# Kernel tuning notes

Hardware: AMD Instinct MI355X
Metric: run time of the kernel (lower is better)

Reference implementation:

```python
import jax, jax.numpy as jnp
import numpy as np

TEMPERATURE = 0.07
MARGIN = 0.15
HARD_NEG_RATIO = 0.5


def setup_inputs() -> dict:
    key = jax.random.key(0)
    k1, k2, k3 = jax.random.split(key, 3)
    B, D = 4096, 128
    drug_emb = jax.random.normal(k1, (B, D), dtype=jnp.float32)
    se_emb = jax.random.normal(k2, (B, D), dtype=jnp.float32)
    # labels spread over [0, 5) so that |diff| > 1.0 negatives exist
    labels = jax.random.uniform(k3, (B,), dtype=jnp.float32) * 5.0
    return {"drug_emb": drug_emb, "se_emb": se_emb, "labels": labels}


def _single_branch_loss(z, labels):
    B = z.shape[0]
    # F.normalize(z, dim=-1): divide by norm clamped to eps
    z = z / jnp.maximum(jnp.linalg.norm(z, axis=-1, keepdims=True), 1e-12)
    sim = jnp.matmul(z, z.T) / TEMPERATURE                      # [B, B]
    label_diff = jnp.abs(labels[None, :] - labels[:, None])     # [B, B]
    self_mask = ~jnp.eye(B, dtype=bool)
    pos_weight = jnp.exp(-label_diff / MARGIN) * self_mask      # soft positives
    neg_mask = (label_diff > 1.0) & self_mask

    # k = max(int(mean per-row negative count * ratio), 1), capped at B-1
    mean_negs = jnp.mean(jnp.sum(neg_mask.astype(jnp.float32), axis=1))
    k = jnp.maximum((mean_negs * HARD_NEG_RATIO).astype(jnp.int32), 1)
    k = jnp.minimum(k, B - 1)

    sim_max = jax.lax.stop_gradient(jnp.max(sim, axis=1, keepdims=True))
    logits = sim - sim_max

    # hard-negative top-k per row, as a static-shape rank test (jit-safe)
    neg_sim = jnp.where(neg_mask, sim, -jnp.inf)
    ranks = jnp.argsort(jnp.argsort(-neg_sim, axis=1), axis=1)  # 0 = largest
    hard_neg_mask = (ranks < k) & neg_mask

    any_neg = jnp.any(neg_mask)
    denom_mask = jnp.where(any_neg, hard_neg_mask | (pos_weight > 0.1), self_mask)

    exp_denom = jnp.sum(jnp.exp(logits) * denom_mask, axis=1, keepdims=True) + 1e-8
    log_prob = logits - jnp.log(exp_denom)
    weighted_log_prob = jnp.sum(pos_weight * log_prob, axis=1)
    denom = jnp.maximum(jnp.sum(pos_weight, axis=1), 1e-8)
    return -jnp.mean(weighted_log_prob / denom)


def reference(drug_emb, se_emb, labels):
    loss_drug = _single_branch_loss(drug_emb, labels)
    loss_se = _single_branch_loss(se_emb, labels)
    loss_cross = _single_branch_loss(drug_emb * se_emb, labels)
    return (loss_drug + loss_se + loss_cross) / 3.0
```

## Files before the change

kernel.cpp:

```cpp
#include <hip/hip_runtime.h>
#include <math.h>

#define BB 4096
#define DD 128
#define KLO 0x3E7FFFFFu
#define KHI 0xC1800000u
#define SH0 19
#define CHUNK 17
#define NBALLOC 4352

typedef __attribute__((ext_vector_type(8))) short bf16x8;
typedef __attribute__((ext_vector_type(4))) float f32x4;

__device__ __forceinline__ unsigned fkey(float x){
    int b = __float_as_int(x);
    return (unsigned)(b ^ ((b >> 31) | 0x80000000));
}
__device__ __forceinline__ float funkey(unsigned u){
    unsigned b = (u & 0x80000000u) ? (u & 0x7fffffffu) : ~u;
    return __uint_as_float(b);
}
__device__ __forceinline__ float bf16f(ushort u){
    return __uint_as_float(((unsigned)u) << 16);
}

__device__ __forceinline__ float blkSumF(float v, volatile float* sh){
    #pragma unroll
    for (int o = 32; o > 0; o >>= 1) v += __shfl_down(v, o);
    int t = threadIdx.x;
    __syncthreads();
    if ((t & 63) == 0) sh[t >> 6] = v;
    __syncthreads();
    return (sh[0] + sh[1]) + (sh[2] + sh[3]);
}

__global__ void krn_normalize(const float* __restrict__ drug, const float* __restrict__ se,
                              const float* __restrict__ labels,
                              ushort* __restrict__ Z,
                              float* __restrict__ wp, float* __restrict__ wm){
    int row = blockIdx.x, br = blockIdx.y, t = threadIdx.x;
    float dv = drug[row * DD + t];
    float sv = se[row * DD + t];
    float v = (br == 0) ? dv : ((br == 1) ? sv : dv * sv);
    float sq = v * v;
    #pragma unroll
    for (int o = 32; o > 0; o >>= 1) sq += __shfl_down(sq, o);
    __shared__ float sh[2];
    if ((t & 63) == 0) sh[t >> 6] = sq;
    __syncthreads();
    float nrm = sqrtf(sh[0] + sh[1]);
    float outv = v / fmaxf(nrm, 1e-12f);
    unsigned u = __float_as_uint(outv);
    unsigned r = (u + 0x7FFFu + ((u >> 16) & 1u)) >> 16;
    int col = t ^ ((row & 7) << 3);
    Z[((size_t)br * BB + row) * DD + col] = (ushort)r;
    if (br == 0 && t == 0){
        float l = labels[row];
        wp[row] = __expf(l * (1.0f / 0.15f));
        wm[row] = __expf(l * (-1.0f / 0.15f));
    }
}

__global__ __launch_bounds__(256) void krn_labelstats(const float* __restrict__ labels,
                                                      int* __restrict__ NC,
                                                      float* __restrict__ PWS,
                                                      int* __restrict__ perm,
                                                      int* __restrict__ ntot){
    __shared__ float lab[BB];
    __shared__ int shi[4], shr[4];
    __shared__ float shf[4];
    int t = threadIdx.x;
    #pragma unroll
    for (int e = 0; e < 4; ++e)
        ((float4*)lab)[t + e * 256] = ((const float4*)labels)[t + e * 256];
    __syncthreads();
    int i0 = blockIdx.x * 16;
    int ctot = 0;
    for (int ii = 0; ii < 16; ++ii){
        int i = i0 + ii;
        float li = lab[i];
        int c = 0, rk = 0;
        float pws = 0.f;
        #pragma unroll
        for (int e = 0; e < 16; ++e){
            int j = t + e * 256;
            float lj = lab[j];
            float d = fabsf(li - lj);
            c += (d > 1.0f) ? 1 : 0;
            pws += __expf(d * (-1.0f / 0.15f));
            rk += (lj < li || (lj == li && j < i)) ? 1 : 0;
        }
        #pragma unroll
        for (int o = 32; o > 0; o >>= 1){
            c += __shfl_down(c, o);
            rk += __shfl_down(rk, o);
            pws += __shfl_down(pws, o);
        }
        __syncthreads();
        if ((t & 63) == 0){ int w = t >> 6; shi[w] = c; shr[w] = rk; shf[w] = pws; }
        __syncthreads();
        if (t == 0){
            int C = (shi[0] + shi[1]) + (shi[2] + shi[3]);
            int R = (shr[0] + shr[1]) + (shr[2] + shr[3]);
            float P = (shf[0] + shf[1]) + (shf[2] + shf[3]);
            NC[i] = C;
            PWS[i] = P - 1.0f;
            perm[R] = i;
            ctot += C;
        }
    }
    if (t == 0) atomicAdd(ntot, ctot);
}

__global__ __launch_bounds__(256) void krn_masks(const float* __restrict__ labels,
                                                 ushort* __restrict__ negmask,
                                                 ushort* __restrict__ posmask){
    __shared__ float lab[BB];
    int t = threadIdx.x;
    #pragma unroll
    for (int e = 0; e < 4; ++e)
        ((float4*)lab)[t + e * 256] = ((const float4*)labels)[t + e * 256];
    __syncthreads();
    float lj[16];
    #pragma unroll
    for (int e = 0; e < 4; ++e)
        #pragma unroll
        for (int c = 0; c < 4; ++c)
            lj[e * 4 + c] = lab[4 * t + 1024 * e + c];
    int i0 = blockIdx.x * 16;
    for (int ii = 0; ii < 16; ++ii){
        int i = i0 + ii;
        float li = lab[i];
        unsigned nb = 0, pb = 0;
        #pragma unroll
        for (int e = 0; e < 4; ++e){
            #pragma unroll
            for (int c = 0; c < 4; ++c){
                int idx = e * 4 + c;
                int j = 4 * t + 1024 * e + c;
                float d = fabsf(li - lj[idx]);
                if (d > 1.0f) nb |= 1u << idx;
                else if (d < 0.34538776f && j != i) pb |= 1u << idx;
            }
        }
        negmask[i * 256 + t] = (ushort)nb;
        posmask[i * 256 + t] = (ushort)pb;
    }
}

__global__ void krn_calck(const int* __restrict__ ntot, int* __restrict__ kflags){
    int N = *ntot;
    int k = N >> 13;
    if (k < 1) k = 1;
    if (k > BB - 1) k = BB - 1;
    kflags[0] = k;
    kflags[1] = (N > 0) ? 1 : 0;
}

__global__ __launch_bounds__(256) void krn_prefix(const ushort* __restrict__ Z,
                                                  const int* __restrict__ perm,
                                                  const float* __restrict__ wp,
                                                  const float* __restrict__ wm,
                                                  float* __restrict__ Yt){
    int d = blockIdx.x, b = blockIdx.y, t = threadIdx.x;
    const ushort* Zb = Z + (size_t)b * BB * DD;
    float uu[16], vv[16], wpj[16], wmj[16];
    float tu = 0.f, tv = 0.f;
    #pragma unroll
    for (int q = 0; q < 16; ++q){
        int r = t * 16 + q;
        int j = perm[r];
        int col = d ^ ((j & 7) << 3);
        float zv = bf16f(Zb[j * DD + col]);
        float a = wp[j], m2 = wm[j];
        wpj[q] = a; wmj[q] = m2;
        uu[q] = a * zv;  vv[q] = m2 * zv;
        tu += uu[q];     tv += vv[q];
    }
    int lane = t & 63, w = t >> 6;
    float xu = tu, xv = tv;
    #pragma unroll
    for (int o = 1; o < 64; o <<= 1){
        float y1 = __shfl_up(xu, o);   if (lane >= o)      xu += y1;
        float y2 = __shfl_down(xv, o); if (lane < 64 - o)  xv += y2;
    }
    __shared__ float wU[4], wV[4];
    if (lane == 63) wU[w] = xu;
    if (lane == 0)  wV[w] = xv;
    __syncthreads();
    float preU = 0.f, sufV = 0.f;
    #pragma unroll
    for (int ww = 0; ww < 4; ++ww){
        if (ww < w) preU += wU[ww];
        if (ww > w) sufV += wV[ww];
    }
    float offU   = preU + (xu - tu);
    float exSufV = sufV + (xv - tv);
    float acc = 0.f;
    #pragma unroll
    for (int q = 15; q >= 0; --q){
        float S = exSufV + acc;
        acc += vv[q];
        vv[q] = S;
    }
    float* ytp = Yt + ((size_t)b * DD + d) * BB + t * 16;
    acc = 0.f;
    #pragma unroll
    for (int q = 0; q < 16; ++q){
        acc += uu[q];
        float P = offU + acc;
        ytp[q] = wmj[q] * P + wpj[q] * vv[q];
    }
}

__global__ __launch_bounds__(256) void krn_psim(const ushort* __restrict__ Z,
                                                const int* __restrict__ perm,
                                                const float* __restrict__ wp,
                                                const float* __restrict__ wm,
                                                const float* __restrict__ Yt,
                                                float* __restrict__ PSIMc){
    int b = blockIdx.y, r0 = blockIdx.x * 32, t = threadIdx.x;
    __shared__ float wt[32][129];
    #pragma unroll
    for (int q = 0; q < 16; ++q){
        int idx = t * 16 + q;
        int d = idx >> 5, r = idx & 31;
        wt[r][d] = Yt[((size_t)b * DD + d) * BB + r0 + r];
    }
    __syncthreads();
    int row = t >> 3, l8 = t & 7;
    int j = perm[r0 + row];
    const ushort* zr = Z + ((size_t)b * BB + j) * DD;
    int swz = (j & 7) << 3;
    float zy = 0.f, zz = 0.f;
    #pragma unroll
    for (int q = 0; q < 16; ++q){
        int d = l8 * 16 + q;
        float zv = bf16f(zr[d ^ swz]);
        float wv = wt[row][d];
        zy = fmaf(zv, wv, zy);
        zz = fmaf(zv, zv, zz);
    }
    #pragma unroll
    for (int o = 1; o < 8; o <<= 1){
        zy += __shfl_xor(zy, o);
        zz += __shfl_xor(zz, o);
    }
    if (l8 == 0)
        PSIMc[(size_t)b * BB + j] = (zy - wp[j] * wm[j] * zz) * (1.0f / 0.07f);
}

__device__ __forceinline__ bf16x8 frag_ld(const ushort* base, int row, int e0){
    int e = e0 ^ ((row & 7) << 3);
    return *(const bf16x8*)(base + row * DD + e);
}

__global__ __launch_bounds__(256) void krn_gemm(const ushort* __restrict__ Z,
                                                float* __restrict__ sim, size_t simStride,
                                                int r0){
    __shared__ ushort As[128 * DD];
    __shared__ ushort Bs[128 * DD];
    const ushort* Zb = Z + (size_t)blockIdx.z * (BB * DD);
    float* simz = sim + (size_t)blockIdx.z * simStride;
    int t = threadIdx.x;
    int rowbase = r0 + blockIdx.y * 128;
    int colbase = blockIdx.x * 128;

    {
        const float4* gA = (const float4*)(Zb + (size_t)rowbase * DD);
        const float4* gB = (const float4*)(Zb + (size_t)colbase * DD);
        float4* lA = (float4*)As;
        float4* lB = (float4*)Bs;
        #pragma unroll
        for (int it = 0; it < 8; ++it){
            lA[it * 256 + t] = gA[it * 256 + t];
            lB[it * 256 + t] = gB[it * 256 + t];
        }
    }
    __syncthreads();

    int wid = t >> 6, lane = t & 63;
    int wr = (wid >> 1) * 64, wc = (wid & 1) * 64;
    int fr = lane & 15, fq = lane >> 4;

    f32x4 acc[4][4];
    #pragma unroll
    for (int m = 0; m < 4; ++m)
        #pragma unroll
        for (int n = 0; n < 4; ++n)
            acc[m][n] = (f32x4){0.f, 0.f, 0.f, 0.f};

    #pragma unroll
    for (int ks = 0; ks < 4; ++ks){
        int e0 = ks * 32 + fq * 8;
        bf16x8 a0 = frag_ld(As, wr + 0 * 16 + fr, e0);
        bf16x8 a1 = frag_ld(As, wr + 1 * 16 + fr, e0);
        bf16x8 a2 = frag_ld(As, wr + 2 * 16 + fr, e0);
        bf16x8 a3 = frag_ld(As, wr + 3 * 16 + fr, e0);
        bf16x8 b0 = frag_ld(Bs, wc + 0 * 16 + fr, e0);
        bf16x8 b1 = frag_ld(Bs, wc + 1 * 16 + fr, e0);
        bf16x8 b2 = frag_ld(Bs, wc + 2 * 16 + fr, e0);
        bf16x8 b3 = frag_ld(Bs, wc + 3 * 16 + fr, e0);
        acc[0][0] = __builtin_amdgcn_mfma_f32_16x16x32_bf16(a0, b0, acc[0][0], 0, 0, 0);
        acc[0][1] = __builtin_amdgcn_mfma_f32_16x16x32_bf16(a0, b1, acc[0][1], 0, 0, 0);
        acc[0][2] = __builtin_amdgcn_mfma_f32_16x16x32_bf16(a0, b2, acc[0][2], 0, 0, 0);
        acc[0][3] = __builtin_amdgcn_mfma_f32_16x16x32_bf16(a0, b3, acc[0][3], 0, 0, 0);
        acc[1][0] = __builtin_amdgcn_mfma_f32_16x16x32_bf16(a1, b0, acc[1][0], 0, 0, 0);
        acc[1][1] = __builtin_amdgcn_mfma_f32_16x16x32_bf16(a1, b1, acc[1][1], 0, 0, 0);
        acc[1][2] = __builtin_amdgcn_mfma_f32_16x16x32_bf16(a1, b2, acc[1][2], 0, 0, 0);
        acc[1][3] = __builtin_amdgcn_mfma_f32_16x16x32_bf16(a1, b3, acc[1][3], 0, 0, 0);
        acc[2][0] = __builtin_amdgcn_mfma_f32_16x16x32_bf16(a2, b0, acc[2][0], 0, 0, 0);
        acc[2][1] = __builtin_amdgcn_mfma_f32_16x16x32_bf16(a2, b1, acc[2][1], 0, 0, 0);
        acc[2][2] = __builtin_amdgcn_mfma_f32_16x16x32_bf16(a2, b2, acc[2][2], 0, 0, 0);
        acc[2][3] = __builtin_amdgcn_mfma_f32_16x16x32_bf16(a2, b3, acc[2][3], 0, 0, 0);
        acc[3][0] = __builtin_amdgcn_mfma_f32_16x16x32_bf16(a3, b0, acc[3][0], 0, 0, 0);
        acc[3][1] = __builtin_amdgcn_mfma_f32_16x16x32_bf16(a3, b1, acc[3][1], 0, 0, 0);
        acc[3][2] = __builtin_amdgcn_mfma_f32_16x16x32_bf16(a3, b2, acc[3][2], 0, 0, 0);
        acc[3][3] = __builtin_amdgcn_mfma_f32_16x16x32_bf16(a3, b3, acc[3][3], 0, 0, 0);
    }

    const float invT = 1.0f / 0.07f;
    int srow0 = blockIdx.y * 128 + wr + fq * 4;
    int scol0 = colbase + wc + fr;
    #pragma unroll
    for (int m = 0; m < 4; ++m){
        #pragma unroll
        for (int n = 0; n < 4; ++n){
            f32x4 c = acc[m][n];
            #pragma unroll
            for (int j = 0; j < 4; ++j)
                simz[(size_t)(srow0 + m * 16 + j) * BB + scol0 + n * 16] = c[j] * invT;
        }
    }
}

__global__ __launch_bounds__(256) void krn_stats(const float* __restrict__ sim, size_t simStride,
                                                 const ushort* __restrict__ negmask,
                                                 const ushort* __restrict__ posmask,
                                                 const int* __restrict__ NCg,
                                                 const float* __restrict__ PWSg,
                                                 const float* __restrict__ PSIMg,
                                                 const int* __restrict__ kflags,
                                                 float* __restrict__ rowloss, int r0){
    __shared__ int hist[NBALLOC];
    __shared__ int wsum[4];
    __shared__ float redf[4];
    __shared__ unsigned selb[3];
    __shared__ unsigned sel2[2];
    __shared__ int cnt;
    __shared__ unsigned list[96];

    int t = threadIdx.x;
    int bi = blockIdx.y;
    int row = blockIdx.x;
    int i = r0 + row;

    #pragma unroll
    for (int e = 0; e < CHUNK; ++e) hist[t + e * 256] = 0;

    unsigned negU = negmask[i * 256 + t];
    unsigned posU = posmask[i * 256 + t];
    const float* srow = sim + (size_t)bi * simStride + (size_t)row * BB;
    const float4* sp = (const float4*)srow;
    float M = srow[i];

    int kk = kflags[0], anyneg = kflags[1];
    int NCv = NCg[i];
    int mode = anyneg ? ((NCv <= kk) ? 1 : 0) : 2;

    float s[16];
    __syncthreads();

    #pragma unroll
    for (int e = 0; e < 4; ++e){
        float4 sv = sp[t + e * 256];
        s[e * 4 + 0] = sv.x; s[e * 4 + 1] = sv.y;
        s[e * 4 + 2] = sv.z; s[e * 4 + 3] = sv.w;
    }
    #pragma unroll
    for (int idx = 0; idx < 16; ++idx)
        if (negU & (1u << idx))
            atomicAdd(&hist[(fkey(s[idx]) - KLO) >> SH0], 1);

    unsigned em = (mode == 2) ? 0xFFFFu : ((mode == 1) ? (negU | posU) : posU);
    float El = 0.f;
    #pragma unroll
    for (int idx = 0; idx < 16; ++idx)
        if (em & (1u << idx)) El += __expf(s[idx] - M);
    __syncthreads();

    unsigned ukth = 0;
    int rfin = 0;
    if (mode == 0){
        unsigned klo = KLO, khi = KHI;
        int sh = SH0;
        int rp = kk;
        bool ready = true;
        while (true){
            if (klo == khi){ ukth = klo; rfin = rp; break; }
            if (!ready){
                #pragma unroll
                for (int e = 0; e < CHUNK; ++e) hist[t + e * 256] = 0;
                __syncthreads();
                #pragma unroll
                for (int idx = 0; idx < 16; ++idx){
                    if (negU & (1u << idx)){
                        unsigned u = fkey(s[idx]);
                        if (u >= klo && u <= khi)
                            atomicAdd(&hist[(u - klo) >> sh], 1);
                    }
                }
                __syncthreads();
            }
            ready = false;
            int g = 255 - t;
            int base = g * CHUNK;
            int ls = 0;
            #pragma unroll
            for (int e = 0; e < CHUNK; ++e) ls += hist[base + e];
            int v = ls;
            #pragma unroll
            for (int o = 1; o < 64; o <<= 1){
                int u2 = __shfl_up(v, o);
                if ((t & 63) >= o) v += u2;
            }
            if ((t & 63) == 63) wsum[t >> 6] = v;
            __syncthreads();
            int w = t >> 6;
            int pre = (w > 0 ? wsum[0] : 0) + (w > 1 ? wsum[1] : 0) + (w > 2 ? wsum[2] : 0);
            v += pre;
            int aec = v - ls;
            if (aec < rp && rp <= v){
                int cum = aec;
                #pragma unroll
                for (int e = CHUNK - 1; e >= 0; --e){
                    int c = hist[base + e];
                    if (cum < rp && rp <= cum + c){
                        selb[0] = (unsigned)(base + e);
                        selb[1] = (unsigned)cum;
                        selb[2] = (unsigned)c;
                        break;
                    }
                    cum += c;
                }
            }
            __syncthreads();
            unsigned B = selb[0];
            int ae = (int)selb[1];
            int c  = (int)selb[2];
            rp -= ae;
            klo += B << sh;
            unsigned nhi = klo + ((1u << sh) - 1u);
            if (nhi < khi) khi = nhi;
            if (c <= 96){
                if (t == 0) cnt = 0;
                __syncthreads();
                #pragma unroll
                for (int idx = 0; idx < 16; ++idx){
                    if (negU & (1u << idx)){
                        unsigned u = fkey(s[idx]);
                        if (u >= klo && u <= khi){
                            int p = atomicAdd(&cnt, 1);
                            list[p] = u;
                        }
                    }
                }
                __syncthreads();
                int cc = cnt;
                if (t < cc){
                    unsigned kj = list[t];
                    int g2 = 0, e2 = 0;
                    for (int mm = 0; mm < cc; ++mm){
                        unsigned km = list[mm];
                        g2 += (km > kj) ? 1 : 0;
                        e2 += (km == kj) ? 1 : 0;
                    }
                    if (g2 < rp && rp <= g2 + e2){ sel2[0] = kj; sel2[1] = (unsigned)g2; }
                }
                __syncthreads();
                ukth = sel2[0];
                rfin = rp - (int)sel2[1];
                break;
            }
            {
                unsigned range = khi - klo;
                int bits = 32 - __clz(range);
                sh = (bits > 12) ? (bits - 12) : 0;
            }
            __syncthreads();
        }
        float skth = funkey(ukth);
        #pragma unroll
        for (int idx = 0; idx < 16; ++idx)
            if ((negU & (1u << idx)) && s[idx] > skth)
                El += __expf(s[idx] - M);
    }

    float Etot = blkSumF(El, redf);

    if (t == 0){
        if (mode == 0) Etot += (float)rfin * __expf(funkey(ukth) - M);
        if (mode == 2) Etot -= 1.0f;
        float PWSc  = PWSg[i];
        float PSIMc = PSIMg[(size_t)bi * BB + i];
        float logE = __logf(Etot + 1e-8f);
        float wl = (PSIMc - M * PWSc) - PWSc * logE;
        rowloss[bi * BB + i] = wl / fmaxf(PWSc, 1e-8f);
    }
}

__global__ void krn_final(const float* __restrict__ rowloss, float* __restrict__ out){
    __shared__ float redf[4];
    int t = threadIdx.x;
    float total = 0.f;
    for (int b = 0; b < 3; ++b){
        float ssum = 0.f;
        for (int e = 0; e < 16; ++e) ssum += rowloss[b * BB + t + e * 256];
        float S = blkSumF(ssum, redf);
        total += S * (1.0f / BB);
    }
    if (t == 0) out[0] = -total / 3.0f;
}

extern "C" void kernel_launch(void* const* d_in, const int* in_sizes, int n_in,
                              void* d_out, int out_size, void* d_ws, size_t ws_size,
                              hipStream_t stream){
    const float* drug   = (const float*)d_in[0];
    const float* se     = (const float*)d_in[1];
    const float* labels = (const float*)d_in[2];
    float* out = (float*)d_out;
    char* ws = (char*)d_ws;

    const size_t zbytes = (size_t)3 * BB * DD * sizeof(ushort);
    const size_t ytbytes = (size_t)3 * DD * BB * sizeof(float);
    const size_t maskbytes = (size_t)BB * 256 * sizeof(ushort);
    const size_t tail = (size_t)(3 + 3 + 1 + 1 + 1 + 1) * BB * sizeof(float)
                      + ytbytes + 2 * maskbytes + 256;

    int slab = BB;
    while (slab > 128 && zbytes + tail + (size_t)3 * slab * BB * sizeof(float) > ws_size)
        slab >>= 1;
    size_t simStride = (size_t)slab * BB;

    ushort* Z      = (ushort*)ws;
    float* simbuf  = (float*)(ws + zbytes);
    size_t off     = zbytes + (size_t)3 * simStride * sizeof(float);
    float* rowloss = (float*)(ws + off);  off += (size_t)3 * BB * sizeof(float);
    float* PSIMc   = (float*)(ws + off);  off += (size_t)3 * BB * sizeof(float);
    float* wp      = (float*)(ws + off);  off += (size_t)BB * sizeof(float);
    float* wm      = (float*)(ws + off);  off += (size_t)BB * sizeof(float);
    float* PWSb    = (float*)(ws + off);  off += (size_t)BB * sizeof(float);
    int*   NCb     = (int*)(ws + off);    off += (size_t)BB * sizeof(int);
    int*   perm    = (int*)(ws + off);    off += (size_t)BB * sizeof(int);
    float* Yt      = (float*)(ws + off);  off += ytbytes;
    ushort* negmask= (ushort*)(ws + off); off += maskbytes;
    ushort* posmask= (ushort*)(ws + off); off += maskbytes;
    int*   ntot    = (int*)(ws + off);
    int*   kflags  = ntot + 2;

    hipMemsetAsync(ntot, 0, 2 * sizeof(int), stream);
    krn_normalize<<<dim3(BB, 3), 128, 0, stream>>>(drug, se, labels, Z, wp, wm);
    krn_labelstats<<<256, 256, 0, stream>>>(labels, NCb, PWSb, perm, ntot);
    krn_masks<<<256, 256, 0, stream>>>(labels, negmask, posmask);
    krn_calck<<<1, 1, 0, stream>>>(ntot, kflags);
    krn_prefix<<<dim3(DD, 3), 256, 0, stream>>>(Z, perm, wp, wm, Yt);
    krn_psim<<<dim3(BB / 32, 3), 256, 0, stream>>>(Z, perm, wp, wm, Yt, PSIMc);

    int nslab = BB / slab;
    for (int s2 = 0; s2 < nslab; ++s2){
        krn_gemm<<<dim3(BB / 128, slab / 128, 3), 256, 0, stream>>>(Z, simbuf, simStride, s2 * slab);
        krn_stats<<<dim3(slab, 3), 256, 0, stream>>>(simbuf, simStride, negmask, posmask,
                                                     NCb, PWSb, PSIMc, kflags, rowloss, s2 * slab);
    }
    krn_final<<<1, 256, 0, stream>>>(rowloss, out);
}
```

Measured before the change: 189.4 us.

## Pre-transpose label-sorted embeddings so prefix scan reads coalesced columns

```diff
diff --git a/kernel.cpp b/kernel.cpp
--- a/kernel.cpp
+++ b/kernel.cpp
@@ -10,6 +10,7 @@
 #define NBALLOC 4352
 
 typedef __attribute__((ext_vector_type(8))) short bf16x8;
+typedef __attribute__((ext_vector_type(8))) unsigned short u16x8;
 typedef __attribute__((ext_vector_type(4))) float f32x4;
 
 __device__ __forceinline__ unsigned fkey(float x){
@@ -37,7 +38,8 @@
 __global__ void krn_normalize(const float* __restrict__ drug, const float* __restrict__ se,
                               const float* __restrict__ labels,
                               ushort* __restrict__ Z,
-                              float* __restrict__ wp, float* __restrict__ wm){
+                              float* __restrict__ wp, float* __restrict__ wm,
+                              float* __restrict__ zzb){
     int row = blockIdx.x, br = blockIdx.y, t = threadIdx.x;
     float dv = drug[row * DD + t];
     float sv = se[row * DD + t];
@@ -46,6 +48,7 @@
     #pragma unroll
     for (int o = 32; o > 0; o >>= 1) sq += __shfl_down(sq, o);
     __shared__ float sh[2];
+    __shared__ float sh2[2];
     if ((t & 63) == 0) sh[t >> 6] = sq;
     __syncthreads();
     float nrm = sqrtf(sh[0] + sh[1]);
@@ -54,6 +57,13 @@
     unsigned r = (u + 0x7FFFu + ((u >> 16) & 1u)) >> 16;
     int col = t ^ ((row & 7) << 3);
     Z[((size_t)br * BB + row) * DD + col] = (ushort)r;
+    float bq = bf16f((ushort)r);
+    float s2 = bq * bq;
+    #pragma unroll
+    for (int o = 32; o > 0; o >>= 1) s2 += __shfl_down(s2, o);
+    if ((t & 63) == 0) sh2[t >> 6] = s2;
+    __syncthreads();
+    if (t == 0) zzb[(size_t)br * BB + row] = sh2[0] + sh2[1];
     if (br == 0 && t == 0){
         float l = labels[row];
         wp[row] = __expf(l * (1.0f / 0.15f));
@@ -157,25 +167,78 @@
     kflags[1] = (N > 0) ? 1 : 0;
 }
 
-__global__ __launch_bounds__(256) void krn_prefix(const ushort* __restrict__ Z,
-                                                  const int* __restrict__ perm,
-                                                  const float* __restrict__ wp,
-                                                  const float* __restrict__ wm,
-                                                  float* __restrict__ Yt){
+__global__ __launch_bounds__(256) void krn_sortz(const ushort* __restrict__ Z,
+                                                 const int* __restrict__ perm,
+                                                 const float* __restrict__ wp,
+                                                 const float* __restrict__ wm,
+                                                 ushort* __restrict__ Zt,
+                                                 float* __restrict__ wps,
+                                                 float* __restrict__ wms){
+    __shared__ ushort tile[64][130];
+    __shared__ int pj[64];
+    int b = blockIdx.y, t = threadIdx.x;
+    int r0 = blockIdx.x * 64;
+    if (t < 64) pj[t] = perm[r0 + t];
+    __syncthreads();
+    if (t < 64 && b == 0){
+        int j = pj[t];
+        wps[r0 + t] = wp[j];
+        wms[r0 + t] = wm[j];
+    }
+    {
+        int rr = t >> 2, q = t & 3;
+        int j = pj[rr];
+        int sw = j & 7;
+        const u16x8* zr = (const u16x8*)(Z + ((size_t)b * BB + j) * DD);
+        #pragma unroll
+        for (int k = 0; k < 4; ++k){
+            int c = q * 4 + k;
+            u16x8 v8 = zr[c ^ sw];
+            #pragma unroll
+            for (int dl = 0; dl < 8; ++dl)
+                tile[rr][c * 8 + dl] = v8[dl];
+        }
+    }
+    __syncthreads();
+    {
+        int d = t >> 1, h = t & 1;
+        ushort* ztp = Zt + ((size_t)b * DD + d) * BB + r0 + h * 32;
+        #pragma unroll
+        for (int g = 0; g < 8; ++g){
+            ushort4 w4;
+            w4.x = tile[h * 32 + g * 4 + 0][d];
+            w4.y = tile[h * 32 + g * 4 + 1][d];
+            w4.z = tile[h * 32 + g * 4 + 2][d];
+            w4.w = tile[h * 32 + g * 4 + 3][d];
+            *(ushort4*)(ztp + g * 4) = w4;
+        }
+    }
+}
+
+__global__ __launch_bounds__(256) void krn_prefix(const ushort* __restrict__ Zt,
+                                                  const float* __restrict__ wps,
+                                                  const float* __restrict__ wms,
+                                                  float* __restrict__ Pt){
     int d = blockIdx.x, b = blockIdx.y, t = threadIdx.x;
-    const ushort* Zb = Z + (size_t)b * BB * DD;
-    float uu[16], vv[16], wpj[16], wmj[16];
+    const ushort* zt = Zt + ((size_t)b * DD + d) * BB;
+    u16x8 z0 = ((const u16x8*)zt)[t * 2];
+    u16x8 z1 = ((const u16x8*)zt)[t * 2 + 1];
+    float zv[16], wpj[16], wmj[16], uu[16], vv[16];
+    #pragma unroll
+    for (int k = 0; k < 4; ++k){
+        float4 a = ((const float4*)wps)[t * 4 + k];
+        float4 m4 = ((const float4*)wms)[t * 4 + k];
+        wpj[k*4+0] = a.x; wpj[k*4+1] = a.y; wpj[k*4+2] = a.z; wpj[k*4+3] = a.w;
+        wmj[k*4+0] = m4.x; wmj[k*4+1] = m4.y; wmj[k*4+2] = m4.z; wmj[k*4+3] = m4.w;
+    }
     float tu = 0.f, tv = 0.f;
     #pragma unroll
     for (int q = 0; q < 16; ++q){
-        int r = t * 16 + q;
-        int j = perm[r];
-        int col = d ^ ((j & 7) << 3);
-        float zv = bf16f(Zb[j * DD + col]);
-        float a = wp[j], m2 = wm[j];
-        wpj[q] = a; wmj[q] = m2;
-        uu[q] = a * zv;  vv[q] = m2 * zv;
-        tu += uu[q];     tv += vv[q];
+        zv[q] = bf16f(q < 8 ? z0[q] : z1[q - 8]);
+        uu[q] = wpj[q] * zv[q];
+        vv[q] = wmj[q] * zv[q];
+        tu += uu[q];
+        tv += vv[q];
     }
     int lane = t & 63, w = t >> 6;
     float xu = tu, xv = tv;
@@ -203,51 +266,31 @@
         acc += vv[q];
         vv[q] = S;
     }
-    float* ytp = Yt + ((size_t)b * DD + d) * BB + t * 16;
+    float* ptp = Pt + ((size_t)b * DD + d) * BB + t * 16;
     acc = 0.f;
     #pragma unroll
     for (int q = 0; q < 16; ++q){
         acc += uu[q];
         float P = offU + acc;
-        ytp[q] = wmj[q] * P + wpj[q] * vv[q];
-    }
-}
-
-__global__ __launch_bounds__(256) void krn_psim(const ushort* __restrict__ Z,
+        ptp[q] = zv[q] * (wmj[q] * P + wpj[q] * vv[q]);
+    }
+}
+
+__global__ __launch_bounds__(256) void krn_psim(const float* __restrict__ Pt,
                                                 const int* __restrict__ perm,
-                                                const float* __restrict__ wp,
-                                                const float* __restrict__ wm,
-                                                const float* __restrict__ Yt,
+                                                const float* __restrict__ wps,
+                                                const float* __restrict__ wms,
+                                                const float* __restrict__ zzb,
                                                 float* __restrict__ PSIMc){
-    int b = blockIdx.y, r0 = blockIdx.x * 32, t = threadIdx.x;
-    __shared__ float wt[32][129];
-    #pragma unroll
-    for (int q = 0; q < 16; ++q){
-        int idx = t * 16 + q;
-        int d = idx >> 5, r = idx & 31;
-        wt[r][d] = Yt[((size_t)b * DD + d) * BB + r0 + r];
-    }
-    __syncthreads();
-    int row = t >> 3, l8 = t & 7;
-    int j = perm[r0 + row];
-    const ushort* zr = Z + ((size_t)b * BB + j) * DD;
-    int swz = (j & 7) << 3;
-    float zy = 0.f, zz = 0.f;
-    #pragma unroll
-    for (int q = 0; q < 16; ++q){
-        int d = l8 * 16 + q;
-        float zv = bf16f(zr[d ^ swz]);
-        float wv = wt[row][d];
-        zy = fmaf(zv, wv, zy);
-        zz = fmaf(zv, zv, zz);
-    }
-    #pragma unroll
-    for (int o = 1; o < 8; o <<= 1){
-        zy += __shfl_xor(zy, o);
-        zz += __shfl_xor(zz, o);
-    }
-    if (l8 == 0)
-        PSIMc[(size_t)b * BB + j] = (zy - wp[j] * wm[j] * zz) * (1.0f / 0.07f);
+    int b = blockIdx.y;
+    int r = blockIdx.x * 256 + threadIdx.x;
+    const float* pt = Pt + (size_t)b * DD * BB + r;
+    float acc = 0.f;
+    #pragma unroll 8
+    for (int d = 0; d < DD; ++d) acc += pt[(size_t)d * BB];
+    int j = perm[r];
+    float self = wps[r] * wms[r] * zzb[(size_t)b * BB + j];
+    PSIMc[(size_t)b * BB + j] = (acc - self) * (1.0f / 0.07f);
 }
 
 __device__ __forceinline__ bf16x8 frag_ld(const ushort* base, int row, int e0){
@@ -531,11 +574,12 @@
     float* out = (float*)d_out;
     char* ws = (char*)d_ws;
 
-    const size_t zbytes = (size_t)3 * BB * DD * sizeof(ushort);
-    const size_t ytbytes = (size_t)3 * DD * BB * sizeof(float);
-    const size_t maskbytes = (size_t)BB * 256 * sizeof(ushort);
-    const size_t tail = (size_t)(3 + 3 + 1 + 1 + 1 + 1) * BB * sizeof(float)
-                      + ytbytes + 2 * maskbytes + 256;
+    const size_t zbytes   = (size_t)3 * BB * DD * sizeof(ushort);
+    const size_t ztbytes  = (size_t)3 * BB * DD * sizeof(ushort);
+    const size_t ptbytes  = (size_t)3 * DD * BB * sizeof(float);
+    const size_t maskbytes= (size_t)BB * 256 * sizeof(ushort);
+    const size_t tail = (size_t)(3 + 3 + 3 + 1 + 1 + 1 + 1 + 1 + 1 + 1) * BB * sizeof(float)
+                      + ztbytes + ptbytes + 2 * maskbytes + 256;
 
     int slab = BB;
     while (slab > 128 && zbytes + tail + (size_t)3 * slab * BB * sizeof(float) > ws_size)
@@ -547,24 +591,29 @@
     size_t off     = zbytes + (size_t)3 * simStride * sizeof(float);
     float* rowloss = (float*)(ws + off);  off += (size_t)3 * BB * sizeof(float);
     float* PSIMc   = (float*)(ws + off);  off += (size_t)3 * BB * sizeof(float);
+    float* zzb     = (float*)(ws + off);  off += (size_t)3 * BB * sizeof(float);
     float* wp      = (float*)(ws + off);  off += (size_t)BB * sizeof(float);
     float* wm      = (float*)(ws + off);  off += (size_t)BB * sizeof(float);
+    float* wps     = (float*)(ws + off);  off += (size_t)BB * sizeof(float);
+    float* wms     = (float*)(ws + off);  off += (size_t)BB * sizeof(float);
     float* PWSb    = (float*)(ws + off);  off += (size_t)BB * sizeof(float);
     int*   NCb     = (int*)(ws + off);    off += (size_t)BB * sizeof(int);
     int*   perm    = (int*)(ws + off);    off += (size_t)BB * sizeof(int);
-    float* Yt      = (float*)(ws + off);  off += ytbytes;
+    ushort* Zt     = (ushort*)(ws + off); off += ztbytes;
+    float* Pt      = (float*)(ws + off);  off += ptbytes;
     ushort* negmask= (ushort*)(ws + off); off += maskbytes;
     ushort* posmask= (ushort*)(ws + off); off += maskbytes;
     int*   ntot    = (int*)(ws + off);
     int*   kflags  = ntot + 2;
 
     hipMemsetAsync(ntot, 0, 2 * sizeof(int), stream);
-    krn_normalize<<<dim3(BB, 3), 128, 0, stream>>>(drug, se, labels, Z, wp, wm);
+    krn_normalize<<<dim3(BB, 3), 128, 0, stream>>>(drug, se, labels, Z, wp, wm, zzb);
     krn_labelstats<<<256, 256, 0, stream>>>(labels, NCb, PWSb, perm, ntot);
     krn_masks<<<256, 256, 0, stream>>>(labels, negmask, posmask);
     krn_calck<<<1, 1, 0, stream>>>(ntot, kflags);
-    krn_prefix<<<dim3(DD, 3), 256, 0, stream>>>(Z, perm, wp, wm, Yt);
-    krn_psim<<<dim3(BB / 32, 3), 256, 0, stream>>>(Z, perm, wp, wm, Yt, PSIMc);
+    krn_sortz<<<dim3(BB / 64, 3), 256, 0, stream>>>(Z, perm, wp, wm, Zt, wps, wms);
+    krn_prefix<<<dim3(DD, 3), 256, 0, stream>>>(Zt, wps, wms, Pt);
+    krn_psim<<<dim3(BB / 256, 3), 256, 0, stream>>>(Pt, perm, wps, wms, zzb, PSIMc);
 
     int nslab = BB / slab;
     for (int s2 = 0; s2 < nslab; ++s2){
```

Result: faster. 181.5 us (-4.2%).
